# Optimization experiments

Hardware: AMD Instinct MI355X
Metric: run time of the kernel (lower is better)

The kernel has to match this reference:

```python
import jax, jax.numpy as jnp
import numpy as np

N = 50000      # nodes
E = 800000     # edges (before self loops)
FE = 256       # expression features
FC = 128       # CNV features
H = 128        # hidden_channels
NC = 8         # num_classes
C = 512        # number of central nodes


def setup_inputs() -> dict:
    key = jax.random.key(0)
    ks = jax.random.split(key, 24)

    def lin(k, fi, fo):
        k1, k2 = jax.random.split(k)
        s = 1.0 / np.sqrt(fi)
        W = jax.random.uniform(k1, (fi, fo), jnp.float32, -s, s)
        b = jax.random.uniform(k2, (fo,), jnp.float32, -s, s)
        return W, b

    x = jax.random.normal(ks[0], (N, FE), jnp.float32)
    c = jax.random.normal(ks[1], (N, FC), jnp.float32)
    edge_index = jax.random.randint(ks[2], (2, E), 0, N, jnp.int32)
    central_idx = jax.random.randint(ks[3], (C,), 0, N, jnp.int32)

    W1e, b1e = lin(ks[4], FE, H)
    W2e, b2e = lin(ks[5], H, H)
    W1c, b1c = lin(ks[6], FC, H)
    W2c, b2c = lin(ks[7], H, H)
    Wm, bm = lin(ks[8], 2 * H, NC)
    Wp1, bp1 = lin(ks[9], NC, H)
    Wp2, bp2 = lin(ks[10], H, NC)

    return dict(
        x=x, c=c, edge_index=edge_index, central_idx=central_idx,
        me_x=jax.random.normal(ks[11], (FE,), jnp.float32),
        me_c=jax.random.normal(ks[12], (FC,), jnp.float32),
        W1e=W1e, b1e=b1e, eps1e=jnp.float32(0.0),
        W2e=W2e, b2e=b2e, eps2e=jnp.float32(0.0),
        W1c=W1c, b1c=b1c, eps1c=jnp.float32(0.0),
        W2c=W2c, b2c=b2c, eps2c=jnp.float32(0.0),
        Wm=Wm, bm=bm, Wp1=Wp1, bp1=bp1, Wp2=Wp2, bp2=bp2,
    )


def _gin_conv(h, src, dst, eps, W, b):
    # GINConv with nn = Linear: lin((1+eps)*x + sum_{j in N(i)} x_j)
    agg = jax.ops.segment_sum(h[src], dst, num_segments=N)  # scatter-add of messages
    return ((1.0 + eps) * h + agg) @ W + b


def reference(x, c, edge_index, central_idx, me_x, me_c,
              W1e, b1e, eps1e, W2e, b2e, eps2e,
              W1c, b1c, eps1c, W2c, b2c, eps2c,
              Wm, bm, Wp1, bp1, Wp2, bp2):
    lrelu = lambda v: jax.nn.leaky_relu(v, 0.2)

    # add self loops
    loops = jnp.arange(N, dtype=edge_index.dtype)
    src = jnp.concatenate([edge_index[0], loops])
    dst = jnp.concatenate([edge_index[1], loops])

    # replace exact-zero entries with learned missing embeddings (broadcast per row)
    x = jnp.where(x == 0, me_x[None, :], x)
    c = jnp.where(c == 0, me_c[None, :], c)

    x_exp = lrelu(_gin_conv(x, src, dst, eps1e, W1e, b1e))
    x_exp = lrelu(_gin_conv(x_exp, src, dst, eps2e, W2e, b2e))

    x_cnv = lrelu(_gin_conv(c, src, dst, eps1c, W1c, b1c))
    x_cnv = lrelu(_gin_conv(x_cnv, src, dst, eps2c, W2c, b2c))

    h = jnp.concatenate([x_exp, x_cnv], axis=1)          # [N, 2H]
    out = lrelu(h @ Wm + bm)                             # [N, NC]

    central = out[central_idx]                           # [C, NC]
    logits = jax.nn.relu(central @ Wp1 + bp1) @ Wp2 + bp2
    return out, logits
```

## Files before the change

kernel.cpp:

```cpp
#include <hip/hip_runtime.h>

typedef unsigned short u16;
typedef __attribute__((ext_vector_type(8))) short short8;
typedef __attribute__((ext_vector_type(4))) float floatx4;

__device__ __forceinline__ float b2f(unsigned int ubits) {
  union { unsigned int i; float f; } cv; cv.i = ubits << 16; return cv.f;
}
__device__ __forceinline__ float hi2f(unsigned int u) {
  union { unsigned int i; float f; } cv; cv.i = u & 0xffff0000u; return cv.f;
}
__device__ __forceinline__ float lo2f(unsigned int u) {
  union { unsigned int i; float f; } cv; cv.i = u << 16; return cv.f;
}
__device__ __forceinline__ u16 f2b(float f) {
  unsigned int u = __builtin_bit_cast(unsigned int, f);
  u += 0x7fffu + ((u >> 16) & 1u);
  return (u16)(u >> 16);
}
__device__ __forceinline__ float lrelu(float v) { return v > 0.f ? v : 0.2f * v; }
__device__ __forceinline__ float rdf(bool isbf, const void* p, int idx) {
  return isbf ? b2f((unsigned int)((const u16*)p)[idx]) : ((const float*)p)[idx];
}

__global__ __launch_bounds__(256) void init_kernel(int* __restrict__ deg, int n,
                                                   const u16* __restrict__ probe,
                                                   int* __restrict__ flag) {
  int i0 = (blockIdx.x * 256 + threadIdx.x) * 4;
  if (i0 + 3 < n) {
    *(int4*)(deg + i0) = make_int4(0, 0, 0, 0);
  } else {
    for (int j = 0; j < 4; j++) if (i0 + j < n) deg[i0 + j] = 0;
  }
  if (blockIdx.x == 0 && threadIdx.x < 64) {
    int lane = threadIdx.x;
    int cnt = 0;
    for (int i = lane; i < 256; i += 64) {
      unsigned int u = probe[i];
      unsigned int e = (u >> 7) & 0xFFu;
      if ((u & 0x7fffu) == 0 || (e >= 60 && e <= 191)) cnt++;
    }
#pragma unroll
    for (int off = 32; off; off >>= 1) cnt += __shfl_down(cnt, off, 64);
    if (lane == 0) *flag = (cnt >= 240) ? 1 : 0;
  }
}

__global__ __launch_bounds__(256) void hist_kernel(const int* __restrict__ dst, int E,
                                                   int* __restrict__ deg) {
  int i = blockIdx.x * 256 + threadIdx.x;
  if (i < E) atomicAdd(deg + dst[i], 1);
}

#define SCB 1024

__global__ __launch_bounds__(256) void scan_phaseA(const int* __restrict__ deg,
                                                   int* __restrict__ bsum, int n) {
  int i0 = blockIdx.x * SCB + threadIdx.x * 4;
  int s = 0;
  if (i0 + 3 < n) {
    int4 v = *(const int4*)(deg + i0);
    s = v.x + v.y + v.z + v.w;
  } else {
    for (int j = 0; j < 4; j++) if (i0 + j < n) s += deg[i0 + j];
  }
#pragma unroll
  for (int off = 32; off; off >>= 1) s += __shfl_down(s, off, 64);
  __shared__ int ws4[4];
  int lane = threadIdx.x & 63, wid = threadIdx.x >> 6;
  if (lane == 0) ws4[wid] = s;
  __syncthreads();
  if (threadIdx.x == 0) bsum[blockIdx.x] = ws4[0] + ws4[1] + ws4[2] + ws4[3];
}

__global__ void scan_phaseB(const int* __restrict__ bsum, int* __restrict__ boff,
                            int PB, int* __restrict__ rowptr, int n) {
  int lane = threadIdx.x;
  int v = (lane < PB) ? bsum[lane] : 0;
  int incl = v;
#pragma unroll
  for (int off = 1; off < 64; off <<= 1) {
    int t = __shfl_up(incl, off, 64);
    if (lane >= off) incl += t;
  }
  if (lane < PB) boff[lane] = incl - v;
  if (lane == 63) rowptr[n] = incl;
}

__global__ __launch_bounds__(256) void scan_phaseC(const int* __restrict__ deg,
                                                   const int* __restrict__ boff,
                                                   int* __restrict__ rowptr,
                                                   int* __restrict__ cursor, int n) {
  int i0 = blockIdx.x * SCB + threadIdx.x * 4;
  int v0 = 0, v1 = 0, v2 = 0, v3 = 0;
  if (i0 + 3 < n) {
    int4 v = *(const int4*)(deg + i0);
    v0 = v.x; v1 = v.y; v2 = v.z; v3 = v.w;
  } else {
    if (i0 < n) v0 = deg[i0];
    if (i0 + 1 < n) v1 = deg[i0 + 1];
    if (i0 + 2 < n) v2 = deg[i0 + 2];
    if (i0 + 3 < n) v3 = deg[i0 + 3];
  }
  int local = v0 + v1 + v2 + v3;
  int lane = threadIdx.x & 63, wid = threadIdx.x >> 6;
  int incl = local;
#pragma unroll
  for (int off = 1; off < 64; off <<= 1) {
    int t = __shfl_up(incl, off, 64);
    if (lane >= off) incl += t;
  }
  __shared__ int ws4[4];
  if (lane == 63) ws4[wid] = incl;
  __syncthreads();
  int woff = 0;
  for (int w = 0; w < wid; w++) woff += ws4[w];
  int run = boff[blockIdx.x] + woff + incl - local;
  if (i0 < n)     { rowptr[i0] = run;     cursor[i0] = run; }     run += v0;
  if (i0 + 1 < n) { rowptr[i0 + 1] = run; cursor[i0 + 1] = run; } run += v1;
  if (i0 + 2 < n) { rowptr[i0 + 2] = run; cursor[i0 + 2] = run; } run += v2;
  if (i0 + 3 < n) { rowptr[i0 + 3] = run; cursor[i0 + 3] = run; }
}

__global__ __launch_bounds__(256) void fill_kernel(const int* __restrict__ src,
                                                   const int* __restrict__ dst, int E,
                                                   int* __restrict__ cursor,
                                                   int* __restrict__ colarr) {
  int i = blockIdx.x * 256 + threadIdx.x;
  if (i < E) {
    int p = atomicAdd(cursor + dst[i], 1);
    colarr[p] = src[i];
  }
}

struct TWDesc {
  const void* W[5];
  int K[5];
  int Nc[5];
  int base[6];
};

__global__ __launch_bounds__(256) void transpose_all(TWDesc d, u16* __restrict__ out,
                                                     const int* __restrict__ flagp) {
  bool isbf = (*flagp != 0);
  int idx = blockIdx.x * 256 + threadIdx.x;
  if (idx >= d.base[5]) return;
  int s = 0;
  while (idx >= d.base[s + 1]) s++;
  int local = idx - d.base[s];
  int K = d.K[s], Nc = d.Nc[s];
  int nn = local / K;
  int k = local - nn * K;
  out[idx] = (nn < Nc) ? f2b(rdf(isbf, d.W[s], k * Nc + nn)) : (u16)0;
}

__device__ __forceinline__ short8 load_a_me(const void* Av, int lda, const void* me,
                                            int r, int k0, int q, bool isbf) {
  short8 a;
  if (isbf) {
    a = *(const short8*)((const u16*)Av + (long)r * lda + k0 + q * 8);
#pragma unroll
    for (int j = 0; j < 8; j++) {
      if (((u16)a[j] & 0x7fffu) == 0)
        a[j] = (short)((const u16*)me)[k0 + q * 8 + j];
    }
  } else {
    const float* A = (const float*)Av;
    const uint4* p = (const uint4*)(A + (long)r * lda + k0 + q * 8);
    uint4 w0 = p[0];
    uint4 w1 = p[1];
    unsigned int ww[8] = {w0.x, w0.y, w0.z, w0.w, w1.x, w1.y, w1.z, w1.w};
#pragma unroll
    for (int j = 0; j < 8; j++) {
      if ((ww[j] & 0x7fffffffu) == 0)
        a[j] = (short)f2b(((const float*)me)[k0 + q * 8 + j]);
      else
        a[j] = (short)((ww[j] + 0x8000u) >> 16);
    }
  }
  return a;
}

__global__ __launch_bounds__(256) void gemm_l1(
    const void* __restrict__ x, const void* __restrict__ cc,
    const void* __restrict__ mex, const void* __restrict__ mec,
    const u16* __restrict__ w1e_t, const u16* __restrict__ w1c_t,
    int M, u16* __restrict__ tb, const int* __restrict__ flagp) {
  bool isbf = (*flagp != 0);
  int wid = threadIdx.x >> 6;
  int lane = threadIdx.x & 63;
  int l15 = lane & 15;
  int q = lane >> 4;
  int row0 = blockIdx.x * 64 + wid * 16;
  int r = row0 + l15;
  if (r >= M) r = M - 1;

  floatx4 acce[8], accc[8];
#pragma unroll
  for (int n = 0; n < 8; n++) { acce[n] = (floatx4){0,0,0,0}; accc[n] = (floatx4){0,0,0,0}; }

  for (int k0 = 0; k0 < 256; k0 += 32) {
    short8 a = load_a_me(x, 256, mex, r, k0, q, isbf);
#pragma unroll
    for (int n = 0; n < 8; n++) {
      short8 b = *(const short8*)(w1e_t + (n * 16 + l15) * 256 + k0 + q * 8);
      acce[n] = __builtin_amdgcn_mfma_f32_16x16x32_bf16(a, b, acce[n], 0, 0, 0);
    }
  }
  for (int k0 = 0; k0 < 128; k0 += 32) {
    short8 a = load_a_me(cc, 128, mec, r, k0, q, isbf);
#pragma unroll
    for (int n = 0; n < 8; n++) {
      short8 b = *(const short8*)(w1c_t + (n * 16 + l15) * 128 + k0 + q * 8);
      accc[n] = __builtin_amdgcn_mfma_f32_16x16x32_bf16(a, b, accc[n], 0, 0, 0);
    }
  }
#pragma unroll
  for (int n = 0; n < 8; n++)
#pragma unroll
    for (int rr = 0; rr < 4; rr++) {
      int row = row0 + q * 4 + rr;
      if (row < M) {
        tb[(long)row * 256 + n * 16 + l15] = f2b(acce[n][rr]);
        tb[(long)row * 256 + 128 + n * 16 + l15] = f2b(accc[n][rr]);
      }
    }
}

__global__ __launch_bounds__(256) void gemm_l2(
    const u16* __restrict__ u,
    const u16* __restrict__ w2e_t, const u16* __restrict__ w2c_t,
    int M, u16* __restrict__ tb) {
  int wid = threadIdx.x >> 6;
  int lane = threadIdx.x & 63;
  int l15 = lane & 15;
  int q = lane >> 4;
  int row0 = blockIdx.x * 64 + wid * 16;
  int r = row0 + l15;
  if (r >= M) r = M - 1;

  floatx4 acce[8], accc[8];
#pragma unroll
  for (int n = 0; n < 8; n++) { acce[n] = (floatx4){0,0,0,0}; accc[n] = (floatx4){0,0,0,0}; }

  for (int k0 = 0; k0 < 128; k0 += 32) {
    short8 ae = *(const short8*)(u + (long)r * 256 + k0 + q * 8);
    short8 ac = *(const short8*)(u + (long)r * 256 + 128 + k0 + q * 8);
#pragma unroll
    for (int n = 0; n < 8; n++) {
      short8 be = *(const short8*)(w2e_t + (n * 16 + l15) * 128 + k0 + q * 8);
      short8 bc = *(const short8*)(w2c_t + (n * 16 + l15) * 128 + k0 + q * 8);
      acce[n] = __builtin_amdgcn_mfma_f32_16x16x32_bf16(ae, be, acce[n], 0, 0, 0);
      accc[n] = __builtin_amdgcn_mfma_f32_16x16x32_bf16(ac, bc, accc[n], 0, 0, 0);
    }
  }
#pragma unroll
  for (int n = 0; n < 8; n++)
#pragma unroll
    for (int rr = 0; rr < 4; rr++) {
      int row = row0 + q * 4 + rr;
      if (row < M) {
        tb[(long)row * 256 + n * 16 + l15] = f2b(acce[n][rr]);
        tb[(long)row * 256 + 128 + n * 16 + l15] = f2b(accc[n][rr]);
      }
    }
}

#define GATHER8                                                         \
  for (; e + 8 <= e1; e += 8) {                                         \
    int c0 = colarr[e], c1 = colarr[e + 1], c2 = colarr[e + 2], c3 = colarr[e + 3]; \
    int c4 = colarr[e + 4], c5 = colarr[e + 5], c6 = colarr[e + 6], c7 = colarr[e + 7]; \
    uint2 p0 = *(const uint2*)(tb + ((long)c0 << 8));                   \
    uint2 p1 = *(const uint2*)(tb + ((long)c1 << 8));                   \
    uint2 p2 = *(const uint2*)(tb + ((long)c2 << 8));                   \
    uint2 p3 = *(const uint2*)(tb + ((long)c3 << 8));                   \
    uint2 p4 = *(const uint2*)(tb + ((long)c4 << 8));                   \
    uint2 p5 = *(const uint2*)(tb + ((long)c5 << 8));                   \
    uint2 p6 = *(const uint2*)(tb + ((long)c6 << 8));                   \
    uint2 p7 = *(const uint2*)(tb + ((long)c7 << 8));                   \
    a0 += lo2f(p0.x); a1 += hi2f(p0.x); a2 += lo2f(p0.y); a3 += hi2f(p0.y); \
    a0 += lo2f(p1.x); a1 += hi2f(p1.x); a2 += lo2f(p1.y); a3 += hi2f(p1.y); \
    a0 += lo2f(p2.x); a1 += hi2f(p2.x); a2 += lo2f(p2.y); a3 += hi2f(p2.y); \
    a0 += lo2f(p3.x); a1 += hi2f(p3.x); a2 += lo2f(p3.y); a3 += hi2f(p3.y); \
    a0 += lo2f(p4.x); a1 += hi2f(p4.x); a2 += lo2f(p4.y); a3 += hi2f(p4.y); \
    a0 += lo2f(p5.x); a1 += hi2f(p5.x); a2 += lo2f(p5.y); a3 += hi2f(p5.y); \
    a0 += lo2f(p6.x); a1 += hi2f(p6.x); a2 += lo2f(p6.y); a3 += hi2f(p6.y); \
    a0 += lo2f(p7.x); a1 += hi2f(p7.x); a2 += lo2f(p7.y); a3 += hi2f(p7.y); \
  }                                                                     \
  for (; e < e1; e++) {                                                 \
    int c = colarr[e];                                                  \
    uint2 p = *(const uint2*)(tb + ((long)c << 8));                     \
    a0 += lo2f(p.x); a1 += hi2f(p.x); a2 += lo2f(p.y); a3 += hi2f(p.y); \
  }

__global__ __launch_bounds__(256) void agg_kernel(
    const u16* __restrict__ t, const int* __restrict__ rowptr, const int* __restrict__ colarr,
    const void* __restrict__ epsE, const void* __restrict__ epsC,
    const void* __restrict__ bE, const void* __restrict__ bC,
    u16* __restrict__ u, int N, const int* __restrict__ flagp) {
  int node = blockIdx.x * 4 + (threadIdx.x >> 6);
  if (node >= N) return;
  bool isbf = (*flagp != 0);
  int lane = threadIdx.x & 63;
  int f0 = lane << 2;
  const u16* tb = t + f0;
  float a0 = 0.f, a1 = 0.f, a2 = 0.f, a3 = 0.f;
  int e = rowptr[node], e1 = rowptr[node + 1];
  GATHER8
  uint2 ps = *(const uint2*)(tb + ((long)node << 8));
  bool isE = (lane < 32);
  float eps2 = 2.0f + rdf(isbf, isE ? epsE : epsC, 0);
  const void* bp = isE ? bE : bC;
  int bi = isE ? f0 : (f0 - 128);
  a0 = lrelu(a0 + eps2 * lo2f(ps.x) + rdf(isbf, bp, bi + 0));
  a1 = lrelu(a1 + eps2 * hi2f(ps.x) + rdf(isbf, bp, bi + 1));
  a2 = lrelu(a2 + eps2 * lo2f(ps.y) + rdf(isbf, bp, bi + 2));
  a3 = lrelu(a3 + eps2 * hi2f(ps.y) + rdf(isbf, bp, bi + 3));
  uint2 o;
  o.x = ((unsigned int)f2b(a1) << 16) | f2b(a0);
  o.y = ((unsigned int)f2b(a3) << 16) | f2b(a2);
  *(uint2*)(u + ((long)node << 8) + f0) = o;
}

__global__ __launch_bounds__(256) void agg_head(
    const u16* __restrict__ t, const int* __restrict__ rowptr, const int* __restrict__ colarr,
    const void* __restrict__ epsE, const void* __restrict__ epsC,
    const void* __restrict__ bE, const void* __restrict__ bC,
    const u16* __restrict__ wm_t, const void* __restrict__ bm,
    float* __restrict__ out, int N, const int* __restrict__ flagp) {
  bool isbf = (*flagp != 0);
  int tid = threadIdx.x;
  int lane = tid & 63;
  int f0 = lane << 2;

  float4 wf[8];
#pragma unroll
  for (int cidx = 0; cidx < 8; cidx++) {
    uint2 w2 = *(const uint2*)(wm_t + cidx * 256 + f0);
    wf[cidx] = make_float4(lo2f(w2.x), hi2f(w2.x), lo2f(w2.y), hi2f(w2.y));
  }

  int node = blockIdx.x * 4 + (tid >> 6);
  if (node >= N) return;
  const u16* tb = t + f0;
  float a0 = 0.f, a1 = 0.f, a2 = 0.f, a3 = 0.f;
  int e = rowptr[node], e1 = rowptr[node + 1];
  GATHER8
  uint2 ps = *(const uint2*)(tb + ((long)node << 8));
  bool isE = (lane < 32);
  float eps2 = 2.0f + rdf(isbf, isE ? epsE : epsC, 0);
  const void* bp = isE ? bE : bC;
  int bi = isE ? f0 : (f0 - 128);
  a0 = lrelu(a0 + eps2 * lo2f(ps.x) + rdf(isbf, bp, bi + 0));
  a1 = lrelu(a1 + eps2 * hi2f(ps.x) + rdf(isbf, bp, bi + 1));
  a2 = lrelu(a2 + eps2 * lo2f(ps.y) + rdf(isbf, bp, bi + 2));
  a3 = lrelu(a3 + eps2 * hi2f(ps.y) + rdf(isbf, bp, bi + 3));

  float p[8];
#pragma unroll
  for (int cidx = 0; cidx < 8; cidx++)
    p[cidx] = a0 * wf[cidx].x + a1 * wf[cidx].y + a2 * wf[cidx].z + a3 * wf[cidx].w;

  float q[4];
#pragma unroll
  for (int cidx = 0; cidx < 4; cidx++) {
    float send = (lane & 32) ? p[cidx] : p[cidx + 4];
    float recv = __shfl_xor(send, 32, 64);
    q[cidx] = ((lane & 32) ? p[cidx + 4] : p[cidx]) + recv;
  }
  float r2[2];
#pragma unroll
  for (int cidx = 0; cidx < 2; cidx++) {
    float send = (lane & 16) ? q[cidx] : q[cidx + 2];
    float recv = __shfl_xor(send, 16, 64);
    r2[cidx] = ((lane & 16) ? q[cidx + 2] : q[cidx]) + recv;
  }
  {
    float send = (lane & 8) ? r2[0] : r2[1];
    float recv = __shfl_xor(send, 8, 64);
    float s = ((lane & 8) ? r2[1] : r2[0]) + recv;
    s += __shfl_xor(s, 4, 64);
    s += __shfl_xor(s, 2, 64);
    s += __shfl_xor(s, 1, 64);
    int col = (lane >> 3) & 7;
    if ((lane & 7) == 0)
      out[(long)node * 8 + col] = lrelu(s + rdf(isbf, bm, col));
  }
}

__global__ __launch_bounds__(128) void mlp_kernel(
    const float* __restrict__ outbuf, const int* __restrict__ central,
    const void* __restrict__ Wp1, const void* __restrict__ bp1,
    const void* __restrict__ Wp2, const void* __restrict__ bp2,
    float* __restrict__ logits, const int* __restrict__ flagp) {
  __shared__ float h1[128];
  __shared__ float o[8];
  bool isbf = (*flagp != 0);
  int b = blockIdx.x, tid = threadIdx.x;
  int node = central[b];
  if (tid < 8) o[tid] = outbuf[node * 8 + tid];
  __syncthreads();
  float s = rdf(isbf, bp1, tid);
#pragma unroll
  for (int k = 0; k < 8; k++) s += o[k] * rdf(isbf, Wp1, k * 128 + tid);
  h1[tid] = fmaxf(s, 0.f);
  __syncthreads();
  if (tid < 8) {
    float s2 = rdf(isbf, bp2, tid);
    for (int k = 0; k < 128; k++) s2 += h1[k] * rdf(isbf, Wp2, k * 8 + tid);
    logits[b * 8 + tid] = s2;
  }
}

extern "C" void kernel_launch(void* const* d_in, const int* in_sizes, int n_in,
                              void* d_out, int out_size, void* d_ws, size_t ws_size,
                              hipStream_t stream) {
  const void* x    = d_in[0];
  const void* c    = d_in[1];
  const int* eidx  = (const int*)d_in[2];
  const int* cidx  = (const int*)d_in[3];
  const void* me_x = d_in[4];
  const void* me_c = d_in[5];
  const void* W1e  = d_in[6];
  const void* b1e  = d_in[7];
  const void* e1e  = d_in[8];
  const void* W2e  = d_in[9];
  const void* b2e  = d_in[10];
  const void* e2e  = d_in[11];
  const void* W1c  = d_in[12];
  const void* b1c  = d_in[13];
  const void* e1c  = d_in[14];
  const void* W2c  = d_in[15];
  const void* b2c  = d_in[16];
  const void* e2c  = d_in[17];
  const void* Wm   = d_in[18];
  const void* bm   = d_in[19];
  const void* Wp1  = d_in[20];
  const void* bp1  = d_in[21];
  const void* Wp2  = d_in[22];
  const void* bp2  = d_in[23];

  const int N = in_sizes[0] / 256;
  const int E = in_sizes[2] / 2;
  const int Cn = in_sizes[3];
  const int* src = eidx;
  const int* dst = eidx + E;

  char* ws = (char*)d_ws;
  int* deg    = (int*)(ws + 0);
  int* rowptr = (int*)(ws + 200192);
  int* cursor = (int*)(ws + 400384);
  int* colarr = (int*)(ws + 600576);
  u16* tbuf   = (u16*)(ws + 3800576);
  u16* ubuf   = (u16*)(ws + 29400576);
  u16* wt_all = (u16*)(ws + 55000576);
  int* flag   = (int*)(ws + 55172608);
  int* bsum   = (int*)(ws + 55172864);
  int* boff   = (int*)(ws + 55173120);

  u16* w1e_t = wt_all + 0;
  u16* w1c_t = wt_all + 32768;
  u16* w2e_t = wt_all + 49152;
  u16* w2c_t = wt_all + 65536;
  u16* wm_t  = wt_all + 81920;

  init_kernel<<<(N + 1023) / 1024, 256, 0, stream>>>(deg, N, (const u16*)x, flag);

  hist_kernel<<<(E + 255) / 256, 256, 0, stream>>>(dst, E, deg);
  int PB = (N + SCB - 1) / SCB;
  scan_phaseA<<<PB, 256, 0, stream>>>(deg, bsum, N);
  scan_phaseB<<<1, 64, 0, stream>>>(bsum, boff, PB, rowptr, N);
  scan_phaseC<<<PB, 256, 0, stream>>>(deg, boff, rowptr, cursor, N);
  fill_kernel<<<(E + 255) / 256, 256, 0, stream>>>(src, dst, E, cursor, colarr);

  TWDesc td;
  td.W[0] = W1e; td.K[0] = 256; td.Nc[0] = 128;
  td.W[1] = W1c; td.K[1] = 128; td.Nc[1] = 128;
  td.W[2] = W2e; td.K[2] = 128; td.Nc[2] = 128;
  td.W[3] = W2c; td.K[3] = 128; td.Nc[3] = 128;
  td.W[4] = Wm;  td.K[4] = 256; td.Nc[4] = 8;
  td.base[0] = 0; td.base[1] = 32768; td.base[2] = 49152;
  td.base[3] = 65536; td.base[4] = 81920; td.base[5] = 86016;
  transpose_all<<<(86016 + 255) / 256, 256, 0, stream>>>(td, wt_all, flag);

  int gb = (N + 63) / 64;
  gemm_l1<<<gb, 256, 0, stream>>>(x, c, me_x, me_c, w1e_t, w1c_t, N, tbuf, flag);
  agg_kernel<<<(N + 3) / 4, 256, 0, stream>>>(tbuf, rowptr, colarr,
      e1e, e1c, b1e, b1c, ubuf, N, flag);
  gemm_l2<<<gb, 256, 0, stream>>>(ubuf, w2e_t, w2c_t, N, tbuf);
  agg_head<<<(N + 3) / 4, 256, 0, stream>>>(tbuf, rowptr, colarr,
      e2e, e2c, b2e, b2c, wm_t, bm, (float*)d_out, N, flag);
  mlp_kernel<<<Cn, 128, 0, stream>>>((const float*)d_out, cidx,
      Wp1, bp1, Wp2, bp2, (float*)d_out + (size_t)N * 8, flag);
}
```

Baseline: 470.0 us.

## Split aggregation into per-half-feature persistent kernels with atomic head accumulation

Aggregation kernels now handle one 128-feature half (expression or CNV) per block, with each lane loading 4 bytes instead of 8. Blocks are persistent, a grid of 2048 striding over 16-node groups, and the block index is arranged so blocks working on the same nodes' halves run close together. The intent is to shrink the gathered row footprint per kernel slice so L2 serves the random gathers better. Because each half now produces only a partial head result, agg2 accumulates it into the output with atomicAdd. This costs a memset of the output, an extra epilogue kernel for bias plus leaky-relu, and atomics on the output.

```diff
diff --git a/kernel.cpp b/kernel.cpp
--- a/kernel.cpp
+++ b/kernel.cpp
@@ -266,126 +266,127 @@
     }
 }
 
-#define GATHER8                                                         \
+#define GATHER8H                                                        \
   for (; e + 8 <= e1; e += 8) {                                         \
     int c0 = colarr[e], c1 = colarr[e + 1], c2 = colarr[e + 2], c3 = colarr[e + 3]; \
     int c4 = colarr[e + 4], c5 = colarr[e + 5], c6 = colarr[e + 6], c7 = colarr[e + 7]; \
-    uint2 p0 = *(const uint2*)(tb + ((long)c0 << 8));                   \
-    uint2 p1 = *(const uint2*)(tb + ((long)c1 << 8));                   \
-    uint2 p2 = *(const uint2*)(tb + ((long)c2 << 8));                   \
-    uint2 p3 = *(const uint2*)(tb + ((long)c3 << 8));                   \
-    uint2 p4 = *(const uint2*)(tb + ((long)c4 << 8));                   \
-    uint2 p5 = *(const uint2*)(tb + ((long)c5 << 8));                   \
-    uint2 p6 = *(const uint2*)(tb + ((long)c6 << 8));                   \
-    uint2 p7 = *(const uint2*)(tb + ((long)c7 << 8));                   \
-    a0 += lo2f(p0.x); a1 += hi2f(p0.x); a2 += lo2f(p0.y); a3 += hi2f(p0.y); \
-    a0 += lo2f(p1.x); a1 += hi2f(p1.x); a2 += lo2f(p1.y); a3 += hi2f(p1.y); \
-    a0 += lo2f(p2.x); a1 += hi2f(p2.x); a2 += lo2f(p2.y); a3 += hi2f(p2.y); \
-    a0 += lo2f(p3.x); a1 += hi2f(p3.x); a2 += lo2f(p3.y); a3 += hi2f(p3.y); \
-    a0 += lo2f(p4.x); a1 += hi2f(p4.x); a2 += lo2f(p4.y); a3 += hi2f(p4.y); \
-    a0 += lo2f(p5.x); a1 += hi2f(p5.x); a2 += lo2f(p5.y); a3 += hi2f(p5.y); \
-    a0 += lo2f(p6.x); a1 += hi2f(p6.x); a2 += lo2f(p6.y); a3 += hi2f(p6.y); \
-    a0 += lo2f(p7.x); a1 += hi2f(p7.x); a2 += lo2f(p7.y); a3 += hi2f(p7.y); \
+    unsigned p0 = *(const unsigned*)(tb + ((long)c0 << 8));             \
+    unsigned p1 = *(const unsigned*)(tb + ((long)c1 << 8));             \
+    unsigned p2 = *(const unsigned*)(tb + ((long)c2 << 8));             \
+    unsigned p3 = *(const unsigned*)(tb + ((long)c3 << 8));             \
+    unsigned p4 = *(const unsigned*)(tb + ((long)c4 << 8));             \
+    unsigned p5 = *(const unsigned*)(tb + ((long)c5 << 8));             \
+    unsigned p6 = *(const unsigned*)(tb + ((long)c6 << 8));             \
+    unsigned p7 = *(const unsigned*)(tb + ((long)c7 << 8));             \
+    a0 += lo2f(p0); a1 += hi2f(p0); a0 += lo2f(p1); a1 += hi2f(p1);     \
+    a0 += lo2f(p2); a1 += hi2f(p2); a0 += lo2f(p3); a1 += hi2f(p3);     \
+    a0 += lo2f(p4); a1 += hi2f(p4); a0 += lo2f(p5); a1 += hi2f(p5);     \
+    a0 += lo2f(p6); a1 += hi2f(p6); a0 += lo2f(p7); a1 += hi2f(p7);     \
   }                                                                     \
   for (; e < e1; e++) {                                                 \
     int c = colarr[e];                                                  \
-    uint2 p = *(const uint2*)(tb + ((long)c << 8));                     \
-    a0 += lo2f(p.x); a1 += hi2f(p.x); a2 += lo2f(p.y); a3 += hi2f(p.y); \
-  }
-
-__global__ __launch_bounds__(256) void agg_kernel(
+    unsigned p = *(const unsigned*)(tb + ((long)c << 8));               \
+    a0 += lo2f(p); a1 += hi2f(p);                                       \
+  }
+
+__global__ __launch_bounds__(256) void agg1_half(
     const u16* __restrict__ t, const int* __restrict__ rowptr, const int* __restrict__ colarr,
     const void* __restrict__ epsE, const void* __restrict__ epsC,
     const void* __restrict__ bE, const void* __restrict__ bC,
-    u16* __restrict__ u, int N, const int* __restrict__ flagp) {
-  int node = blockIdx.x * 4 + (threadIdx.x >> 6);
-  if (node >= N) return;
+    u16* __restrict__ u, int N, int ngroups, const int* __restrict__ flagp) {
   bool isbf = (*flagp != 0);
-  int lane = threadIdx.x & 63;
-  int f0 = lane << 2;
-  const u16* tb = t + f0;
-  float a0 = 0.f, a1 = 0.f, a2 = 0.f, a3 = 0.f;
-  int e = rowptr[node], e1 = rowptr[node + 1];
-  GATHER8
-  uint2 ps = *(const uint2*)(tb + ((long)node << 8));
-  bool isE = (lane < 32);
-  float eps2 = 2.0f + rdf(isbf, isE ? epsE : epsC, 0);
-  const void* bp = isE ? bE : bC;
-  int bi = isE ? f0 : (f0 - 128);
-  a0 = lrelu(a0 + eps2 * lo2f(ps.x) + rdf(isbf, bp, bi + 0));
-  a1 = lrelu(a1 + eps2 * hi2f(ps.x) + rdf(isbf, bp, bi + 1));
-  a2 = lrelu(a2 + eps2 * lo2f(ps.y) + rdf(isbf, bp, bi + 2));
-  a3 = lrelu(a3 + eps2 * hi2f(ps.y) + rdf(isbf, bp, bi + 3));
-  uint2 o;
-  o.x = ((unsigned int)f2b(a1) << 16) | f2b(a0);
-  o.y = ((unsigned int)f2b(a3) << 16) | f2b(a2);
-  *(uint2*)(u + ((long)node << 8) + f0) = o;
-}
-
-__global__ __launch_bounds__(256) void agg_head(
+  int b = blockIdx.x;
+  int h = (b >> 2) & 1;
+  int quad = b & 3;
+  int wid = threadIdx.x >> 6, lane = threadIdx.x & 63;
+  int f = h * 128 + lane * 2;
+  const u16* tb = t + f;
+  float eps2 = 2.0f + rdf(isbf, h ? epsC : epsE, 0);
+  const void* bp = h ? bC : bE;
+  int bi = h ? (f - 128) : f;
+  float bb0 = rdf(isbf, bp, bi);
+  float bb1 = rdf(isbf, bp, bi + 1);
+  int gstride = gridDim.x >> 3;
+  for (int g = b >> 3; g < ngroups; g += gstride) {
+    int node = g * 16 + quad * 4 + wid;
+    if (node >= N) continue;
+    float a0 = 0.f, a1 = 0.f;
+    int e = rowptr[node], e1 = rowptr[node + 1];
+    GATHER8H
+    unsigned ps = *(const unsigned*)(tb + ((long)node << 8));
+    a0 = lrelu(a0 + eps2 * lo2f(ps) + bb0);
+    a1 = lrelu(a1 + eps2 * hi2f(ps) + bb1);
+    *(unsigned*)(u + ((long)node << 8) + f) = ((unsigned)f2b(a1) << 16) | f2b(a0);
+  }
+}
+
+__global__ __launch_bounds__(256) void agg2_half(
     const u16* __restrict__ t, const int* __restrict__ rowptr, const int* __restrict__ colarr,
     const void* __restrict__ epsE, const void* __restrict__ epsC,
     const void* __restrict__ bE, const void* __restrict__ bC,
-    const u16* __restrict__ wm_t, const void* __restrict__ bm,
-    float* __restrict__ out, int N, const int* __restrict__ flagp) {
+    const u16* __restrict__ wm_t, float* __restrict__ out,
+    int N, int ngroups, const int* __restrict__ flagp) {
   bool isbf = (*flagp != 0);
-  int tid = threadIdx.x;
-  int lane = tid & 63;
-  int f0 = lane << 2;
-
-  float4 wf[8];
-#pragma unroll
-  for (int cidx = 0; cidx < 8; cidx++) {
-    uint2 w2 = *(const uint2*)(wm_t + cidx * 256 + f0);
-    wf[cidx] = make_float4(lo2f(w2.x), hi2f(w2.x), lo2f(w2.y), hi2f(w2.y));
-  }
-
-  int node = blockIdx.x * 4 + (tid >> 6);
-  if (node >= N) return;
-  const u16* tb = t + f0;
-  float a0 = 0.f, a1 = 0.f, a2 = 0.f, a3 = 0.f;
-  int e = rowptr[node], e1 = rowptr[node + 1];
-  GATHER8
-  uint2 ps = *(const uint2*)(tb + ((long)node << 8));
-  bool isE = (lane < 32);
-  float eps2 = 2.0f + rdf(isbf, isE ? epsE : epsC, 0);
-  const void* bp = isE ? bE : bC;
-  int bi = isE ? f0 : (f0 - 128);
-  a0 = lrelu(a0 + eps2 * lo2f(ps.x) + rdf(isbf, bp, bi + 0));
-  a1 = lrelu(a1 + eps2 * hi2f(ps.x) + rdf(isbf, bp, bi + 1));
-  a2 = lrelu(a2 + eps2 * lo2f(ps.y) + rdf(isbf, bp, bi + 2));
-  a3 = lrelu(a3 + eps2 * hi2f(ps.y) + rdf(isbf, bp, bi + 3));
-
-  float p[8];
-#pragma unroll
-  for (int cidx = 0; cidx < 8; cidx++)
-    p[cidx] = a0 * wf[cidx].x + a1 * wf[cidx].y + a2 * wf[cidx].z + a3 * wf[cidx].w;
-
-  float q[4];
-#pragma unroll
-  for (int cidx = 0; cidx < 4; cidx++) {
-    float send = (lane & 32) ? p[cidx] : p[cidx + 4];
-    float recv = __shfl_xor(send, 32, 64);
-    q[cidx] = ((lane & 32) ? p[cidx + 4] : p[cidx]) + recv;
-  }
-  float r2[2];
-#pragma unroll
-  for (int cidx = 0; cidx < 2; cidx++) {
-    float send = (lane & 16) ? q[cidx] : q[cidx + 2];
-    float recv = __shfl_xor(send, 16, 64);
-    r2[cidx] = ((lane & 16) ? q[cidx + 2] : q[cidx]) + recv;
-  }
-  {
+  int b = blockIdx.x;
+  int h = (b >> 2) & 1;
+  int quad = b & 3;
+  int wid = threadIdx.x >> 6, lane = threadIdx.x & 63;
+  int f = h * 128 + lane * 2;
+  const u16* tb = t + f;
+  float eps2 = 2.0f + rdf(isbf, h ? epsC : epsE, 0);
+  const void* bp = h ? bC : bE;
+  int bi = h ? (f - 128) : f;
+  float bb0 = rdf(isbf, bp, bi);
+  float bb1 = rdf(isbf, bp, bi + 1);
+  float2 wf[8];
+#pragma unroll
+  for (int cc = 0; cc < 8; cc++) {
+    unsigned w = *(const unsigned*)(wm_t + cc * 256 + f);
+    wf[cc] = make_float2(lo2f(w), hi2f(w));
+  }
+  int gstride = gridDim.x >> 3;
+  for (int g = b >> 3; g < ngroups; g += gstride) {
+    int node = g * 16 + quad * 4 + wid;
+    if (node >= N) continue;
+    float a0 = 0.f, a1 = 0.f;
+    int e = rowptr[node], e1 = rowptr[node + 1];
+    GATHER8H
+    unsigned ps = *(const unsigned*)(tb + ((long)node << 8));
+    a0 = lrelu(a0 + eps2 * lo2f(ps) + bb0);
+    a1 = lrelu(a1 + eps2 * hi2f(ps) + bb1);
+    float p[8];
+#pragma unroll
+    for (int cc = 0; cc < 8; cc++) p[cc] = a0 * wf[cc].x + a1 * wf[cc].y;
+    float q[4];
+#pragma unroll
+    for (int cc = 0; cc < 4; cc++) {
+      float send = (lane & 32) ? p[cc] : p[cc + 4];
+      float recv = __shfl_xor(send, 32, 64);
+      q[cc] = ((lane & 32) ? p[cc + 4] : p[cc]) + recv;
+    }
+    float r2[2];
+#pragma unroll
+    for (int cc = 0; cc < 2; cc++) {
+      float send = (lane & 16) ? q[cc] : q[cc + 2];
+      float recv = __shfl_xor(send, 16, 64);
+      r2[cc] = ((lane & 16) ? q[cc + 2] : q[cc]) + recv;
+    }
     float send = (lane & 8) ? r2[0] : r2[1];
     float recv = __shfl_xor(send, 8, 64);
     float s = ((lane & 8) ? r2[1] : r2[0]) + recv;
     s += __shfl_xor(s, 4, 64);
     s += __shfl_xor(s, 2, 64);
     s += __shfl_xor(s, 1, 64);
-    int col = (lane >> 3) & 7;
     if ((lane & 7) == 0)
-      out[(long)node * 8 + col] = lrelu(s + rdf(isbf, bm, col));
-  }
+      atomicAdd(out + (long)node * 8 + ((lane >> 3) & 7), s);
+  }
+}
+
+__global__ __launch_bounds__(256) void head_epi(float* __restrict__ out, const void* __restrict__ bm,
+                                                int total, const int* __restrict__ flagp) {
+  bool isbf = (*flagp != 0);
+  int i = blockIdx.x * 256 + threadIdx.x;
+  if (i < total) out[i] = lrelu(out[i] + rdf(isbf, bm, i & 7));
 }
 
 __global__ __launch_bounds__(128) void mlp_kernel(
@@ -464,6 +465,8 @@
   u16* w2c_t = wt_all + 65536;
   u16* wm_t  = wt_all + 81920;
 
+  hipMemsetAsync(d_out, 0, (size_t)N * 8 * sizeof(float), stream);
+
   init_kernel<<<(N + 1023) / 1024, 256, 0, stream>>>(deg, N, (const u16*)x, flag);
 
   hist_kernel<<<(E + 255) / 256, 256, 0, stream>>>(dst, E, deg);
@@ -484,12 +487,14 @@
   transpose_all<<<(86016 + 255) / 256, 256, 0, stream>>>(td, wt_all, flag);
 
   int gb = (N + 63) / 64;
+  int ngroups = (N + 15) / 16;
   gemm_l1<<<gb, 256, 0, stream>>>(x, c, me_x, me_c, w1e_t, w1c_t, N, tbuf, flag);
-  agg_kernel<<<(N + 3) / 4, 256, 0, stream>>>(tbuf, rowptr, colarr,
-      e1e, e1c, b1e, b1c, ubuf, N, flag);
+  agg1_half<<<2048, 256, 0, stream>>>(tbuf, rowptr, colarr,
+      e1e, e1c, b1e, b1c, ubuf, N, ngroups, flag);
   gemm_l2<<<gb, 256, 0, stream>>>(ubuf, w2e_t, w2c_t, N, tbuf);
-  agg_head<<<(N + 3) / 4, 256, 0, stream>>>(tbuf, rowptr, colarr,
-      e2e, e2c, b2e, b2c, wm_t, bm, (float*)d_out, N, flag);
+  agg2_half<<<2048, 256, 0, stream>>>(tbuf, rowptr, colarr,
+      e2e, e2c, b2e, b2c, wm_t, (float*)d_out, N, ngroups, flag);
+  head_epi<<<(N * 8 + 255) / 256, 256, 0, stream>>>((float*)d_out, bm, N * 8, flag);
   mlp_kernel<<<Cn, 128, 0, stream>>>((const float*)d_out, cidx,
       Wp1, bp1, Wp2, bp2, (float*)d_out + (size_t)N * 8, flag);
 }
```

Result: slower. 482.0 us (+2.5%).
